# Kernel tuning notes

Measured on AMD Instinct MI355X. Metric: run time of the kernel, lower is better.

Reference implementation:

```python
import jax, jax.numpy as jnp
import numpy as np

N, K = 16384, 16
SIZE, DIST = 256, 64
HEADS, ATTN = 8, 32
HIDDEN = 512
HA = HEADS * ATTN  # 256
EDGE = SIZE + DIST  # key/value input size per edge


def setup_inputs() -> dict:
    key = jax.random.key(0)
    ks = jax.random.split(key, 16)
    s = lambda k, fi, fo: jax.random.normal(k, (fi, fo), jnp.float32) / np.sqrt(fi)
    return {
        "features": jax.random.normal(ks[0], (N, SIZE), jnp.float32),
        "distances": jax.random.normal(ks[1], (N, K, DIST), jnp.float32),
        "structure": jax.random.randint(ks[2], (N, K), 0, N, jnp.int32),
        # local MLP: size -> hidden -> hidden -> size (depth=3 linears)
        "W0": s(ks[3], SIZE, HIDDEN), "b0": jnp.zeros((HIDDEN,), jnp.float32),
        "W1": s(ks[4], HIDDEN, HIDDEN), "b1": jnp.zeros((HIDDEN,), jnp.float32),
        "W2": s(ks[5], HIDDEN, SIZE), "b2": jnp.zeros((SIZE,), jnp.float32),
        # neighbour dot multi-head attention
        "Wq": s(ks[6], SIZE, HA), "bq": jnp.zeros((HA,), jnp.float32),
        "Wk": s(ks[7], EDGE, HA), "bk": jnp.zeros((HA,), jnp.float32),
        "Wv": s(ks[8], EDGE, HA), "bv": jnp.zeros((HA,), jnp.float32),
        "Wo": s(ks[9], HA, SIZE), "bo": jnp.zeros((SIZE,), jnp.float32),
    }


def reference(features, distances, structure,
              W0, b0, W1, b1, W2, b2,
              Wq, bq, Wk, bk, Wv, bv, Wo, bo):
    # batch_norm=False -> bn layers are identity; activation = relu
    inputs = jax.nn.relu(features)                      # [N, size]
    # local MLP (ReLU between layers), then outer activation
    h = jax.nn.relu(inputs @ W0 + b0)
    h = jax.nn.relu(h @ W1 + b1)
    local = jax.nn.relu(h @ W2 + b2)                    # [N, size]
    # edge structure: gather neighbour features, concat distance features
    neigh = local[structure]                            # [N, K, size]
    edge = jnp.concatenate([neigh, distances], axis=-1) # [N, K, size+dist]
    # neighbour-restricted multi-head dot attention
    q = (features @ Wq + bq).reshape(N, HEADS, ATTN)    # [N, H, A]
    k = (edge @ Wk + bk).reshape(N, K, HEADS, ATTN)     # [N, K, H, A]
    v = (edge @ Wv + bv).reshape(N, K, HEADS, ATTN)
    scale = jnp.float32(1.0 / np.sqrt(ATTN))
    scores = jnp.einsum('nha,nkha->nhk', q, k) * scale  # [N, H, K]
    attn = jax.nn.softmax(scores, axis=-1)
    o = jnp.einsum('nhk,nkha->nha', attn, v).reshape(N, HA)
    out = o @ Wo + bo                                   # [N, size]
    return features + out
```

## Files before the change

kernel.cpp:

```cpp
#include <hip/hip_runtime.h>
#include <hip/hip_bf16.h>

#define NN 16384
#define SIZE 256
#define DISTD 64
#define KNBR 16
#define HEADS 8
#define HIDDEN 512
#define HA 256
#define SCALE 0.17677669529663687f

typedef __bf16 bf16;
typedef bf16 bf16x2 __attribute__((ext_vector_type(2)));
typedef bf16 bf16x4 __attribute__((ext_vector_type(4)));
typedef bf16 bf16x8 __attribute__((ext_vector_type(8)));
typedef float f32x4 __attribute__((ext_vector_type(4)));

__device__ __forceinline__ void gload16(const void* g, void* l) {
    __builtin_amdgcn_global_load_lds(
        (const __attribute__((address_space(1))) unsigned int*)g,
        (__attribute__((address_space(3))) unsigned int*)l, 16, 0, 0);
}

template<bool BIAS, bool RELU_OUT, bool RESID, typename OutT, int SUBS>
__global__ __launch_bounds__(256) void gemm128(
    const bf16* __restrict__ A, const bf16* __restrict__ BT,
    const float* __restrict__ bias, const float* __restrict__ resid,
    OutT* __restrict__ C, int M, int N, int K)
{
    __shared__ alignas(16) bf16 As[2][SUBS][128][32];
    __shared__ alignas(16) bf16 Bs[2][SUBS][128][32];

    const int t = threadIdx.x;
    const int w = t >> 6, l = t & 63;
    const int bm = blockIdx.y * 128, bn = blockIdx.x * 128;
    const int wr = (w >> 1) * 64, wc = (w & 1) * 64;
    const int BK = 32 * SUBS;

    f32x4 acc[4][4] = {};

    const bf16* ag = A  + (size_t)(bm + (t >> 2)) * K + (t & 3) * 8;
    const bf16* bg = BT + (size_t)(bn + (t >> 2)) * K + (t & 3) * 8;

    auto STAGE = [&](int buf, int k0) {
        #pragma unroll
        for (int s = 0; s < SUBS; ++s) {
            bf16* asl = &As[buf][s][w << 4][0];
            bf16* bsl = &Bs[buf][s][w << 4][0];
            gload16(ag + k0 + s * 32, asl);
            gload16(ag + k0 + s * 32 + (size_t)64 * K, (char*)asl + 4096);
            gload16(bg + k0 + s * 32, bsl);
            gload16(bg + k0 + s * 32 + (size_t)64 * K, (char*)bsl + 4096);
        }
    };

    const int nt = K / BK;
    STAGE(0, 0);
    __syncthreads();

    for (int tt = 0; tt < nt; ++tt) {
        const int cur = tt & 1;
        if (tt + 1 < nt) STAGE(cur ^ 1, (tt + 1) * BK);

        #pragma unroll
        for (int s = 0; s < SUBS; ++s) {
            bf16x8 af[4], bfr[4];
            #pragma unroll
            for (int m = 0; m < 4; ++m)
                af[m] = *(const bf16x8*)&As[cur][s][wr + m * 16 + (l & 15)][(l >> 4) * 8];
            #pragma unroll
            for (int n2 = 0; n2 < 4; ++n2)
                bfr[n2] = *(const bf16x8*)&Bs[cur][s][wc + n2 * 16 + (l & 15)][(l >> 4) * 8];
            #pragma unroll
            for (int m = 0; m < 4; ++m)
                #pragma unroll
                for (int n2 = 0; n2 < 4; ++n2)
                    acc[m][n2] = __builtin_amdgcn_mfma_f32_16x16x32_bf16(
                        af[m], bfr[n2], acc[m][n2], 0, 0, 0);
        }
        __syncthreads();
    }

    #pragma unroll
    for (int m = 0; m < 4; ++m) {
        const int row = bm + wr + m * 16 + ((l >> 4) << 2);
        #pragma unroll
        for (int n2 = 0; n2 < 4; ++n2) {
            const int col = bn + wc + n2 * 16 + (l & 15);
            #pragma unroll
            for (int i = 0; i < 4; ++i) {
                float v = acc[m][n2][i];
                if (BIAS) v += bias[col];
                if (RESID) v += resid[(size_t)(row + i) * N + col];
                if (RELU_OUT) v = fmaxf(v, 0.f);
                C[(size_t)(row + i) * N + col] = (OutT)v;
            }
        }
    }
}

__global__ __launch_bounds__(256) void g1qcat_kernel(
    const bf16* __restrict__ fbf, const bf16* __restrict__ frbf,
    const bf16* __restrict__ W0T, const float* __restrict__ b0,
    const bf16* __restrict__ WqcatT, const float* __restrict__ bqcat,
    bf16* __restrict__ H0, bf16* __restrict__ qcat)
{
    __shared__ alignas(16) bf16 As[2][128][32];
    __shared__ alignas(16) bf16 Bs[2][128][32];

    const int bx = blockIdx.x, by = blockIdx.y;
    const bool isG1 = bx < 4;
    const int cx = bx - 4;
    const bf16* A  = isG1 ? frbf : fbf;
    const bf16* BT = isG1 ? (W0T + (size_t)bx * 128 * 256)
                          : (WqcatT + (size_t)cx * 128 * 256);
    const float* bias = isG1 ? (b0 + bx * 128) : (bqcat + cx * 128);
    const int K = 256;

    const int t = threadIdx.x;
    const int w = t >> 6, l = t & 63;
    const int bm = by * 128;
    const int wr = (w >> 1) * 64, wc = (w & 1) * 64;

    f32x4 acc[4][4] = {};

    const bf16* ag = A  + (size_t)(bm + (t >> 2)) * K + (t & 3) * 8;
    const bf16* bg = BT + (size_t)(t >> 2) * K + (t & 3) * 8;

    {
        bf16* asl = &As[0][w << 4][0];
        bf16* bsl = &Bs[0][w << 4][0];
        gload16(ag, asl);
        gload16(ag + (size_t)64 * K, (char*)asl + 4096);
        gload16(bg, bsl);
        gload16(bg + (size_t)64 * K, (char*)bsl + 4096);
    }
    __syncthreads();

    for (int tt = 0; tt < 8; ++tt) {
        const int cur = tt & 1;
        if (tt + 1 < 8) {
            const int k0 = (tt + 1) << 5;
            bf16* asl = &As[cur ^ 1][w << 4][0];
            bf16* bsl = &Bs[cur ^ 1][w << 4][0];
            gload16(ag + k0, asl);
            gload16(ag + k0 + (size_t)64 * K, (char*)asl + 4096);
            gload16(bg + k0, bsl);
            gload16(bg + k0 + (size_t)64 * K, (char*)bsl + 4096);
        }
        bf16x8 af[4], bfr[4];
        #pragma unroll
        for (int m = 0; m < 4; ++m)
            af[m] = *(const bf16x8*)&As[cur][wr + m * 16 + (l & 15)][(l >> 4) * 8];
        #pragma unroll
        for (int n2 = 0; n2 < 4; ++n2)
            bfr[n2] = *(const bf16x8*)&Bs[cur][wc + n2 * 16 + (l & 15)][(l >> 4) * 8];
        #pragma unroll
        for (int m = 0; m < 4; ++m)
            #pragma unroll
            for (int n2 = 0; n2 < 4; ++n2)
                acc[m][n2] = __builtin_amdgcn_mfma_f32_16x16x32_bf16(
                    af[m], bfr[n2], acc[m][n2], 0, 0, 0);
        __syncthreads();
    }

    #pragma unroll
    for (int m = 0; m < 4; ++m) {
        const int lrow = wr + m * 16 + ((l >> 4) << 2);
        #pragma unroll
        for (int n2 = 0; n2 < 4; ++n2) {
            const int lcol = wc + n2 * 16 + (l & 15);
            #pragma unroll
            for (int i = 0; i < 4; ++i) {
                float v = acc[m][n2][i] + bias[lcol];
                const size_t row = bm + lrow + i;
                if (isG1) {
                    H0[row * 512 + bx * 128 + lcol] = (bf16)fmaxf(v, 0.f);
                } else {
                    qcat[row * 768 + cx * 128 + lcol] = (bf16)v;
                }
            }
        }
    }
}

__global__ __launch_bounds__(256) void prep_all(
    const float* __restrict__ features,
    const float* __restrict__ W0, const float* __restrict__ W1,
    const float* __restrict__ W2, const float* __restrict__ Wq,
    const float* __restrict__ bq, const float* __restrict__ Wk,
    const float* __restrict__ Wv, const float* __restrict__ Wo,
    const float* __restrict__ bo, const float* __restrict__ bv,
    bf16* __restrict__ fbf, bf16* __restrict__ frbf,
    bf16* __restrict__ W0T, bf16* __restrict__ W1T, bf16* __restrict__ W2T,
    bf16* __restrict__ WkvT, bf16* __restrict__ WqcatT, bf16* __restrict__ WstackT,
    float* __restrict__ bqcat, float* __restrict__ biaso)
{
    if (blockIdx.x < 4096) {
        int id = blockIdx.x * 256 + threadIdx.x;
        float4 v = ((const float4*)features)[id];
        bf16x4 a, r;
        a[0] = (bf16)v.x; a[1] = (bf16)v.y; a[2] = (bf16)v.z; a[3] = (bf16)v.w;
        r[0] = (bf16)fmaxf(v.x, 0.f); r[1] = (bf16)fmaxf(v.y, 0.f);
        r[2] = (bf16)fmaxf(v.z, 0.f); r[3] = (bf16)fmaxf(v.w, 0.f);
        ((bf16x4*)fbf)[id] = a; ((bf16x4*)frbf)[id] = r;
        return;
    }
    long id = (blockIdx.x - 4096) * 256L + threadIdx.x;
    if (id < 131072) {
        int n = id >> 8, k = id & 255;
        W0T[id] = (bf16)W0[(long)k * 512 + n]; return;
    }
    id -= 131072;
    if (id < 262144) {
        int n = id >> 9, k = id & 511;
        W1T[id] = (bf16)W1[(long)k * 512 + n]; return;
    }
    id -= 262144;
    if (id < 131072) {
        int n = id >> 9, k = id & 511;
        W2T[id] = (bf16)W2[(long)k * 256 + n]; return;
    }
    id -= 131072;
    if (id < 131072) {
        int n = id >> 8, k = id & 255;
        WkvT[id] = (bf16)(n < 256 ? Wk[(long)k * 256 + n] : Wv[(long)k * 256 + (n - 256)]);
        return;
    }
    id -= 131072;
    if (id < 196608) {
        int col = id >> 8, c = id & 255;
        float s;
        if (col < 256) s = Wq[(long)c * 256 + col];
        else {
            int hd = col - 256, h = hd >> 6, d = hd & 63;
            s = 0.f;
            #pragma unroll
            for (int a = 0; a < 32; ++a)
                s += Wq[(long)c * 256 + h * 32 + a] * Wk[(long)(256 + d) * 256 + h * 32 + a];
        }
        WqcatT[id] = (bf16)(s * SCALE); return;
    }
    id -= 196608;
    if (id < 196608) {
        int col = (int)(id / 768), r = (int)(id % 768);
        float s;
        if (r < 256) s = Wo[(long)r * 256 + col];
        else {
            int hd = r - 256, h = hd >> 6, d = hd & 63;
            s = 0.f;
            #pragma unroll
            for (int a = 0; a < 32; ++a)
                s += Wv[(long)(256 + d) * 256 + h * 32 + a] * Wo[(long)(h * 32 + a) * 256 + col];
        }
        WstackT[id] = (bf16)s; return;
    }
    id -= 196608;
    if (id < 768) {
        float s;
        if (id < 256) s = bq[id];
        else {
            int hd = (int)id - 256, h = hd >> 6, d = hd & 63;
            s = 0.f;
            #pragma unroll
            for (int a = 0; a < 32; ++a)
                s += bq[h * 32 + a] * Wk[(long)(256 + d) * 256 + h * 32 + a];
        }
        bqcat[id] = s * SCALE; return;
    }
    id -= 768;
    if (id < 256) {
        float s = bo[id];
        for (int u = 0; u < 256; ++u) s += bv[u] * Wo[(long)u * 256 + id];
        biaso[id] = s;
    }
}

__global__ __launch_bounds__(256) void attn_kernel(
    const bf16* __restrict__ qcat,
    const bf16* __restrict__ localKV,
    const float* __restrict__ dist,
    const int*  __restrict__ structure,
    bf16* __restrict__ concat)
{
    const int n = blockIdx.x;
    const int t = threadIdx.x;
    const int h = t >> 5, j = (t >> 1) & 15, part = t & 1;

    __shared__ float dist_s[16][68];
    __shared__ bf16  V_s[16][264];
    __shared__ float attn_s[8][16];
    __shared__ int   s_s[16];

    {
        const float* dp = dist + (long)n * (KNBR * DISTD);
        #pragma unroll
        for (int i = 0; i < 4; ++i) {
            int e = i * 256 + t;
            dist_s[e >> 6][e & 63] = dp[e];
        }
    }
    if (t < 16) s_s[t] = structure[(long)n * KNBR + t];
    __syncthreads();

    #pragma unroll
    for (int pass = 0; pass < 2; ++pass) {
        int idx = pass * 256 + t;
        int row = idx >> 5, chunk = idx & 31;
        bf16x8 v = *(const bf16x8*)(localKV + (long)s_s[row] * 512 + 256 + chunk * 8);
        *(bf16x8*)&V_s[row][chunk * 8] = v;
    }

    const bf16* qp_q = qcat + (long)n * 768 + h * 32 + part * 16;
    bf16x8 qa = *(const bf16x8*)qp_q;
    bf16x8 qb = *(const bf16x8*)(qp_q + 8);
    const bf16* qp_p = qcat + (long)n * 768 + 256 + h * 64 + part * 32;
    bf16x8 p0 = *(const bf16x8*)qp_p;
    bf16x8 p1 = *(const bf16x8*)(qp_p + 8);
    bf16x8 p2 = *(const bf16x8*)(qp_p + 16);
    bf16x8 p3 = *(const bf16x8*)(qp_p + 24);
    const bf16* kp = localKV + (long)s_s[j] * 512 + h * 32 + part * 16;
    bf16x8 ka = *(const bf16x8*)kp;
    bf16x8 kb = *(const bf16x8*)(kp + 8);

    float sc = 0.f;
    #pragma unroll
    for (int i = 0; i < 8; ++i)
        sc += (float)qa[i] * (float)ka[i] + (float)qb[i] * (float)kb[i];

    const int dbase = part * 32;
    #pragma unroll
    for (int i = 0; i < 8; ++i) sc += dist_s[j][dbase + i]      * (float)p0[i];
    #pragma unroll
    for (int i = 0; i < 8; ++i) sc += dist_s[j][dbase + 8 + i]  * (float)p1[i];
    #pragma unroll
    for (int i = 0; i < 8; ++i) sc += dist_s[j][dbase + 16 + i] * (float)p2[i];
    #pragma unroll
    for (int i = 0; i < 8; ++i) sc += dist_s[j][dbase + 24 + i] * (float)p3[i];

    sc += __shfl_xor(sc, 1);
    float m = sc;
    m = fmaxf(m, __shfl_xor(m, 2));
    m = fmaxf(m, __shfl_xor(m, 4));
    m = fmaxf(m, __shfl_xor(m, 8));
    m = fmaxf(m, __shfl_xor(m, 16));
    float e = __expf(sc - m);
    float sum = e;
    sum += __shfl_xor(sum, 2);
    sum += __shfl_xor(sum, 4);
    sum += __shfl_xor(sum, 8);
    sum += __shfl_xor(sum, 16);
    float attn = e / sum;
    if (!part) attn_s[h][j] = attn;
    __syncthreads();

    if (t < 128) {
        const int c0 = t * 2;
        const int hh = t >> 4;
        float a0 = 0.f, a1 = 0.f;
        #pragma unroll
        for (int j2 = 0; j2 < 16; ++j2) {
            float wgt = attn_s[hh][j2];
            bf16x2 pv = *(const bf16x2*)&V_s[j2][c0];
            a0 += wgt * (float)pv[0];
            a1 += wgt * (float)pv[1];
        }
        bf16x2 o2; o2[0] = (bf16)a0; o2[1] = (bf16)a1;
        *(bf16x2*)&concat[(long)n * 768 + c0] = o2;
    } else {
        const int u = t - 128;
        const int base = u * 4;
        const int h3 = u >> 4, d3 = (u & 15) * 4;
        f32x4 acc4 = {};
        #pragma unroll
        for (int j2 = 0; j2 < 16; ++j2) {
            float wgt = attn_s[h3][j2];
            const f32x4 dv = *(const f32x4*)&dist_s[j2][d3];
            acc4 += wgt * dv;
        }
        bf16x4 o4;
        #pragma unroll
        for (int i = 0; i < 4; ++i) o4[i] = (bf16)acc4[i];
        *(bf16x4*)&concat[(long)n * 768 + 256 + base] = o4;
    }
}

extern "C" void kernel_launch(void* const* d_in, const int* in_sizes, int n_in,
                              void* d_out, int out_size, void* d_ws, size_t ws_size,
                              hipStream_t stream)
{
    const float* features = (const float*)d_in[0];
    const float* dist     = (const float*)d_in[1];
    const int*   structure= (const int*)d_in[2];
    const float* W0 = (const float*)d_in[3];
    const float* b0 = (const float*)d_in[4];
    const float* W1 = (const float*)d_in[5];
    const float* b1 = (const float*)d_in[6];
    const float* W2 = (const float*)d_in[7];
    const float* b2 = (const float*)d_in[8];
    const float* Wq = (const float*)d_in[9];
    const float* bq = (const float*)d_in[10];
    const float* Wk = (const float*)d_in[11];
    const float* Wv = (const float*)d_in[13];
    const float* bv = (const float*)d_in[14];
    const float* Wo = (const float*)d_in[15];
    const float* bo = (const float*)d_in[16];
    float* out = (float*)d_out;

    const size_t MB = 1u << 20;
    char* w = (char*)d_ws;
    bf16*  fbf     = (bf16*)(w + 0 * MB);
    bf16*  local_b = (bf16*)(w + 0 * MB);
    bf16*  frbf    = (bf16*)(w + 8 * MB);
    bf16*  localKV = (bf16*)(w + 8 * MB);
    bf16*  H0      = (bf16*)(w + 16 * MB);
    bf16*  qcat    = (bf16*)(w + 32 * MB);
    bf16*  H1      = (bf16*)(w + 56 * MB);
    bf16*  concat  = (bf16*)(w + 56 * MB);
    char*  wb      = w + 80 * MB;
    bf16*  W0T     = (bf16*)(wb + 0);
    bf16*  W1T     = (bf16*)(wb + 262144);
    bf16*  W2T     = (bf16*)(wb + 786432);
    bf16*  WkvT    = (bf16*)(wb + 1048576);
    bf16*  WqcatT  = (bf16*)(wb + 1310720);
    bf16*  WstackT = (bf16*)(wb + 1703936);
    float* bqcat   = (float*)(wb + 2097152);
    float* biaso   = (float*)(wb + 2100224);

    dim3 blk(256);

    prep_all<<<dim3(8196), blk, 0, stream>>>(
        features, W0, W1, W2, Wq, bq, Wk, Wv, Wo, bo, bv,
        fbf, frbf, W0T, W1T, W2T, WkvT, WqcatT, WstackT, bqcat, biaso);

    g1qcat_kernel<<<dim3(10, 128), blk, 0, stream>>>(
        fbf, frbf, W0T, b0, WqcatT, bqcat, H0, qcat);

    gemm128<true,  true,  false, bf16, 2><<<dim3(4, 128), blk, 0, stream>>>(
        H0, W1T, b1, nullptr, H1, NN, 512, 512);
    gemm128<true,  true,  false, bf16, 2><<<dim3(2, 128), blk, 0, stream>>>(
        H1, W2T, b2, nullptr, local_b, NN, 256, 512);
    gemm128<false, false, false, bf16, 2><<<dim3(4, 128), blk, 0, stream>>>(
        local_b, WkvT, nullptr, nullptr, localKV, NN, 512, 256);

    attn_kernel<<<dim3(NN), blk, 0, stream>>>(
        qcat, localKV, dist, structure, concat);

    gemm128<true,  false, true,  float, 2><<<dim3(2, 128), blk, 0, stream>>>(
        concat, WstackT, biaso, features, out, NN, 256, 768);
}
```

Before: 162.1 us.

## Tile weight transposes through LDS and load V directly into registers

The weight-preparation kernel now transposes each weight matrix in 32x32 tiles staged through shared memory, so global reads and writes are both coalesced instead of strided per element. The fused Wq·Wk and Wv·Wo products are split into their own block ranges, which shrinks the launch grid. In the attention kernel, V rows are no longer staged in shared memory: each of the first 128 threads loads its 16 bf16 pairs straight from global memory into registers, and the distance dot product uses vector LDS reads. Per-thread V loads are narrower (4 bytes each) and raise register pressure.

```diff
diff --git a/kernel.cpp b/kernel.cpp
--- a/kernel.cpp
+++ b/kernel.cpp
@@ -196,8 +196,11 @@
     bf16* __restrict__ WkvT, bf16* __restrict__ WqcatT, bf16* __restrict__ WstackT,
     float* __restrict__ bqcat, float* __restrict__ biaso)
 {
+    __shared__ float tl[32][33];
+    const int t = threadIdx.x;
+
     if (blockIdx.x < 4096) {
-        int id = blockIdx.x * 256 + threadIdx.x;
+        int id = blockIdx.x * 256 + t;
         float4 v = ((const float4*)features)[id];
         bf16x4 a, r;
         a[0] = (bf16)v.x; a[1] = (bf16)v.y; a[2] = (bf16)v.z; a[3] = (bf16)v.w;
@@ -206,73 +209,75 @@
         ((bf16x4*)fbf)[id] = a; ((bf16x4*)frbf)[id] = r;
         return;
     }
-    long id = (blockIdx.x - 4096) * 256L + threadIdx.x;
-    if (id < 131072) {
-        int n = id >> 8, k = id & 255;
-        W0T[id] = (bf16)W0[(long)k * 512 + n]; return;
-    }
-    id -= 131072;
-    if (id < 262144) {
-        int n = id >> 9, k = id & 511;
-        W1T[id] = (bf16)W1[(long)k * 512 + n]; return;
-    }
-    id -= 262144;
-    if (id < 131072) {
-        int n = id >> 9, k = id & 511;
-        W2T[id] = (bf16)W2[(long)k * 256 + n]; return;
-    }
-    id -= 131072;
-    if (id < 131072) {
-        int n = id >> 8, k = id & 255;
-        WkvT[id] = (bf16)(n < 256 ? Wk[(long)k * 256 + n] : Wv[(long)k * 256 + (n - 256)]);
+    if (blockIdx.x < 4864) {
+        int tile = blockIdx.x - 4096;
+        const float* src; bf16* dst; int srcLd, dstLd, tpr; float scl = 1.f;
+        if (tile < 128)      { src = W0; srcLd = 512; tpr = 16; dst = W0T;  dstLd = 256; }
+        else if (tile < 384) { tile -= 128; src = W1; srcLd = 512; tpr = 16; dst = W1T;  dstLd = 512; }
+        else if (tile < 512) { tile -= 384; src = W2; srcLd = 256; tpr = 8;  dst = W2T;  dstLd = 512; }
+        else if (tile < 576) { tile -= 512; src = Wk; srcLd = 256; tpr = 8;  dst = WkvT; dstLd = 256; }
+        else if (tile < 640) { tile -= 576; src = Wv; srcLd = 256; tpr = 8;  dst = WkvT + 65536; dstLd = 256; }
+        else if (tile < 704) { tile -= 640; src = Wq; srcLd = 256; tpr = 8;  dst = WqcatT; dstLd = 256; scl = SCALE; }
+        else                 { tile -= 704; src = Wo; srcLd = 256; tpr = 8;  dst = WstackT; dstLd = 768; }
+        const int tr = tile / tpr, tc = tile % tpr;
+        const int x = t & 31, y0 = t >> 5;
+        #pragma unroll
+        for (int p = 0; p < 4; ++p) {
+            int y = y0 + 8 * p;
+            tl[y][x] = src[(size_t)(tr * 32 + y) * srcLd + tc * 32 + x];
+        }
+        __syncthreads();
+        #pragma unroll
+        for (int p = 0; p < 4; ++p) {
+            int a2 = y0 + 8 * p;
+            dst[(size_t)(tc * 32 + a2) * dstLd + tr * 32 + x] = (bf16)(tl[x][a2] * scl);
+        }
         return;
     }
-    id -= 131072;
-    if (id < 196608) {
-        int col = id >> 8, c = id & 255;
-        float s;
-        if (col < 256) s = Wq[(long)c * 256 + col];
-        else {
-            int hd = col - 256, h = hd >> 6, d = hd & 63;
-            s = 0.f;
-            #pragma unroll
-            for (int a = 0; a < 32; ++a)
-                s += Wq[(long)c * 256 + h * 32 + a] * Wk[(long)(256 + d) * 256 + h * 32 + a];
-        }
-        WqcatT[id] = (bf16)(s * SCALE); return;
-    }
-    id -= 196608;
-    if (id < 196608) {
-        int col = (int)(id / 768), r = (int)(id % 768);
-        float s;
-        if (r < 256) s = Wo[(long)r * 256 + col];
-        else {
-            int hd = r - 256, h = hd >> 6, d = hd & 63;
-            s = 0.f;
-            #pragma unroll
-            for (int a = 0; a < 32; ++a)
-                s += Wv[(long)(256 + d) * 256 + h * 32 + a] * Wo[(long)(h * 32 + a) * 256 + col];
-        }
-        WstackT[id] = (bf16)s; return;
-    }
-    id -= 196608;
-    if (id < 768) {
-        float s;
-        if (id < 256) s = bq[id];
-        else {
-            int hd = (int)id - 256, h = hd >> 6, d = hd & 63;
-            s = 0.f;
-            #pragma unroll
-            for (int a = 0; a < 32; ++a)
-                s += bq[h * 32 + a] * Wk[(long)(256 + d) * 256 + h * 32 + a];
-        }
-        bqcat[id] = s * SCALE; return;
-    }
-    id -= 768;
-    if (id < 256) {
-        float s = bo[id];
-        for (int u = 0; u < 256; ++u) s += bv[u] * Wo[(long)u * 256 + id];
-        biaso[id] = s;
+    if (blockIdx.x < 5376) {
+        int id = (blockIdx.x - 4864) * 256 + t;
+        int hd = id >> 8, c = id & 255;
+        int h = hd >> 6, d = hd & 63;
+        float s = 0.f;
+        #pragma unroll
+        for (int a = 0; a < 32; ++a)
+            s += Wq[(size_t)c * 256 + h * 32 + a] * Wk[(size_t)(256 + d) * 256 + h * 32 + a];
+        WqcatT[65536 + id] = (bf16)(s * SCALE);
+        return;
+    }
+    if (blockIdx.x < 5888) {
+        int id = (blockIdx.x - 5376) * 256 + t;
+        int r2 = id >> 8, col = id & 255;
+        int h = r2 >> 6, d = r2 & 63;
+        float s = 0.f;
+        #pragma unroll
+        for (int a = 0; a < 32; ++a)
+            s += Wv[(size_t)(256 + d) * 256 + h * 32 + a] * Wo[(size_t)(h * 32 + a) * 256 + col];
+        WstackT[(size_t)col * 768 + 256 + r2] = (bf16)s;
+        return;
+    }
+    if (blockIdx.x == 5888) {
+        #pragma unroll
+        for (int rep = 0; rep < 3; ++rep) {
+            int idx = rep * 256 + t;
+            if (idx >= 768) break;
+            float s;
+            if (idx < 256) s = bq[idx];
+            else {
+                int hd = idx - 256, h = hd >> 6, d = hd & 63;
+                s = 0.f;
+                #pragma unroll
+                for (int a = 0; a < 32; ++a)
+                    s += bq[h * 32 + a] * Wk[(size_t)(256 + d) * 256 + h * 32 + a];
+            }
+            bqcat[idx] = s * SCALE;
+        }
+        return;
+    }
+    {
+        float s = bo[t];
+        for (int u = 0; u < 256; ++u) s += bv[u] * Wo[(size_t)u * 256 + t];
+        biaso[t] = s;
     }
 }
 
@@ -288,7 +293,6 @@
     const int h = t >> 5, j = (t >> 1) & 15, part = t & 1;
 
     __shared__ float dist_s[16][68];
-    __shared__ bf16  V_s[16][264];
     __shared__ float attn_s[8][16];
     __shared__ int   s_s[16];
 
@@ -303,22 +307,23 @@
     if (t < 16) s_s[t] = structure[(long)n * KNBR + t];
     __syncthreads();
 
-    #pragma unroll
-    for (int pass = 0; pass < 2; ++pass) {
-        int idx = pass * 256 + t;
-        int row = idx >> 5, chunk = idx & 31;
-        bf16x8 v = *(const bf16x8*)(localKV + (long)s_s[row] * 512 + 256 + chunk * 8);
-        *(bf16x8*)&V_s[row][chunk * 8] = v;
+    bf16x2 pv[16];
+    const int c0 = (t & 127) * 2;
+    if (t < 128) {
+        #pragma unroll
+        for (int j2 = 0; j2 < 16; ++j2)
+            pv[j2] = *(const bf16x2*)(localKV + (size_t)s_s[j2] * 512 + 256 + c0);
     }
 
     const bf16* qp_q = qcat + (long)n * 768 + h * 32 + part * 16;
     bf16x8 qa = *(const bf16x8*)qp_q;
     bf16x8 qb = *(const bf16x8*)(qp_q + 8);
     const bf16* qp_p = qcat + (long)n * 768 + 256 + h * 64 + part * 32;
-    bf16x8 p0 = *(const bf16x8*)qp_p;
-    bf16x8 p1 = *(const bf16x8*)(qp_p + 8);
-    bf16x8 p2 = *(const bf16x8*)(qp_p + 16);
-    bf16x8 p3 = *(const bf16x8*)(qp_p + 24);
+    bf16x8 p[4];
+    p[0] = *(const bf16x8*)qp_p;
+    p[1] = *(const bf16x8*)(qp_p + 8);
+    p[2] = *(const bf16x8*)(qp_p + 16);
+    p[3] = *(const bf16x8*)(qp_p + 24);
     const bf16* kp = localKV + (long)s_s[j] * 512 + h * 32 + part * 16;
     bf16x8 ka = *(const bf16x8*)kp;
     bf16x8 kb = *(const bf16x8*)(kp + 8);
@@ -330,13 +335,14 @@
 
     const int dbase = part * 32;
     #pragma unroll
-    for (int i = 0; i < 8; ++i) sc += dist_s[j][dbase + i]      * (float)p0[i];
-    #pragma unroll
-    for (int i = 0; i < 8; ++i) sc += dist_s[j][dbase + 8 + i]  * (float)p1[i];
-    #pragma unroll
-    for (int i = 0; i < 8; ++i) sc += dist_s[j][dbase + 16 + i] * (float)p2[i];
-    #pragma unroll
-    for (int i = 0; i < 8; ++i) sc += dist_s[j][dbase + 24 + i] * (float)p3[i];
+    for (int i = 0; i < 4; ++i) {
+        const f32x4 a4 = *(const f32x4*)&dist_s[j][dbase + 8 * i];
+        const f32x4 b4 = *(const f32x4*)&dist_s[j][dbase + 8 * i + 4];
+        sc += a4[0] * (float)p[i][0] + a4[1] * (float)p[i][1]
+            + a4[2] * (float)p[i][2] + a4[3] * (float)p[i][3]
+            + b4[0] * (float)p[i][4] + b4[1] * (float)p[i][5]
+            + b4[2] * (float)p[i][6] + b4[3] * (float)p[i][7];
+    }
 
     sc += __shfl_xor(sc, 1);
     float m = sc;
@@ -355,15 +361,13 @@
     __syncthreads();
 
     if (t < 128) {
-        const int c0 = t * 2;
         const int hh = t >> 4;
         float a0 = 0.f, a1 = 0.f;
         #pragma unroll
         for (int j2 = 0; j2 < 16; ++j2) {
             float wgt = attn_s[hh][j2];
-            bf16x2 pv = *(const bf16x2*)&V_s[j2][c0];
-            a0 += wgt * (float)pv[0];
-            a1 += wgt * (float)pv[1];
+            a0 += wgt * (float)pv[j2][0];
+            a1 += wgt * (float)pv[j2][1];
         }
         bf16x2 o2; o2[0] = (bf16)a0; o2[1] = (bf16)a1;
         *(bf16x2*)&concat[(long)n * 768 + c0] = o2;
@@ -429,7 +433,7 @@
 
     dim3 blk(256);
 
-    prep_all<<<dim3(8196), blk, 0, stream>>>(
+    prep_all<<<dim3(5890), blk, 0, stream>>>(
         features, W0, W1, W2, Wq, bq, Wk, Wv, Wo, bo, bv,
         fbf, frbf, W0T, W1T, W2T, WkvT, WqcatT, WstackT, bqcat, biaso);
 
```

New measurement: 164.0 us. No clear change (+1.1%).
